# Performance work log

Measured on AMD Instinct MI355X. Metric: run time of the kernel, lower is better.

The kernel has to match this reference:

```python
import jax, jax.numpy as jnp
import numpy as np

I16_MIN, I16_MAX = -32768, 32767
NUM_SEG = 8


def setup_inputs() -> dict:
    key = jax.random.key(0)
    k1, k2, k3, k4, k5, k6 = jax.random.split(key, 6)
    # Float activation; quantized to qint16 inside the op via input_scale.
    x = jax.random.normal(k1, (16, 1024, 2048), dtype=jnp.float32)
    input_scale = jnp.full((1,), 1.0 / 8192.0, dtype=jnp.float32)  # randn*8192 spans most of int16
    out_scale = jnp.full((1,), 1e-3, dtype=jnp.float32)
    # Per-segment fixed-point linear coefficients (as produced by _convert_linear_kb / toqint):
    # 16-bit k, wide b pre-shifted by left_shift, result right-shifted by right_shift.
    alpha = jax.random.randint(k2, (NUM_SEG,), -4096, 4096, dtype=jnp.int32)        # int16 k
    beta = jax.random.randint(k3, (NUM_SEG,), -(1 << 20), 1 << 20, dtype=jnp.int32)  # int b
    left_shift = jax.random.randint(k4, (NUM_SEG,), 0, 5, dtype=jnp.int32)           # int8 shift
    right_shift = jax.random.randint(k5, (NUM_SEG,), 1, 15, dtype=jnp.int32)         # int8 shift
    # Sorted segment upper bounds in quantized domain; last entry pinned to qint16 max
    # (mirrors `segment_max[-1] = info.max` in _init_multi_table_params).
    segment_max = jnp.sort(jax.random.randint(k6, (NUM_SEG,), I16_MIN, I16_MAX, dtype=jnp.int32))
    segment_max = segment_max.at[-1].set(I16_MAX)
    return dict(x=x, input_scale=input_scale, out_scale=out_scale, alpha=alpha,
                beta=beta, left_shift=left_shift, right_shift=right_shift,
                segment_max=segment_max)


def reference(x, input_scale, out_scale, alpha, beta, left_shift, right_shift, segment_max):
    # Quantize input to qint16 (scale-only, zero_point = 0 as in the module).
    xi = jnp.clip(jnp.round(x / input_scale), I16_MIN, I16_MAX).astype(jnp.int32)
    # Segment selection: element belongs to the first segment whose upper bound >= xi.
    idx = jnp.clip(jnp.searchsorted(segment_max, xi, side='left'), 0, NUM_SEG - 1)
    # Gather per-segment fixed-point coefficients.
    k = alpha[idx]
    b = beta[idx]
    ls = left_shift[idx]
    rs = right_shift[idx]
    # Hardware shift-multiply-add: acc = k*x + (b << left_shift), then rounded
    # arithmetic right shift by right_shift, saturate to qint16.
    acc = k * xi + jnp.left_shift(b, ls)
    round_bias = jnp.where(rs > 0, jnp.left_shift(jnp.int32(1), jnp.maximum(rs - 1, 0)), jnp.int32(0))
    qy = jnp.clip(jnp.right_shift(acc + round_bias, rs), I16_MIN, I16_MAX)
    # Dequantized output (QTensor data * out_scale, zero_point = 0).
    return qy.astype(jnp.float32) * out_scale
```

## Files before the change

### kernel.cpp

```cpp
#include <hip/hip_runtime.h>


typedef float f32x4 __attribute__((ext_vector_type(4)));

__device__ __forceinline__ float seg_one(float x, float inv_s,
                                         float sm0, float sm1, float sm2, float sm3,
                                         float sm4, float sm5, float sm6,
                                         const float2* tab, float olo, float ohi)
{
    float xf = rintf(x * inv_s);
    xf = __builtin_amdgcn_fmed3f(xf, -32768.0f, 32767.0f);
    int idx = (sm0 < xf) + (sm1 < xf) + (sm2 < xf) + (sm3 < xf)
            + (sm4 < xf) + (sm5 < xf) + (sm6 < xf);
    float2 t = tab[idx];
    float y = fmaf(t.x, xf, t.y);
    return __builtin_amdgcn_fmed3f(y, olo, ohi);
}

__global__ __launch_bounds__(256) void SegmentLUT_83021717831949_kernel(
    const float* __restrict__ x,
    const float* __restrict__ input_scale,
    const float* __restrict__ out_scale,
    const int*   __restrict__ alpha,
    const int*   __restrict__ beta,
    const int*   __restrict__ lsh,
    const int*   __restrict__ rsh,
    const int*   __restrict__ smax,
    float*       __restrict__ out,
    int n)
{
    int nvec = n >> 2;
    int i = (int)(blockIdx.x * blockDim.x + threadIdx.x);
    bool valid = i < nvec;

    const f32x4* __restrict__ xv = (const f32x4*)x;
    f32x4 v = {};
    if (valid) v = xv[i];

    __shared__ float2 tab[8];
    float os = out_scale[0];
    if (threadIdx.x < 8) {
        int j  = (int)threadIdx.x;
        int rs = rsh[j];
        int rm1 = rs - 1 > 0 ? rs - 1 : 0;
        int rbias = rs > 0 ? (1 << rm1) : 0;
        int bc = (int)((unsigned)beta[j] << (lsh[j] & 31)) + rbias;
        float sc = ldexpf(os, -rs);
        tab[j] = make_float2((float)alpha[j] * sc, (float)bc * sc);
    }
    float inv_s = 1.0f / input_scale[0];
    float sm0 = (float)smax[0], sm1 = (float)smax[1], sm2 = (float)smax[2];
    float sm3 = (float)smax[3], sm4 = (float)smax[4], sm5 = (float)smax[5];
    float sm6 = (float)smax[6];
    float olo = -32768.0f * os, ohi = 32767.0f * os;
    __syncthreads();

    if (valid) {
        f32x4 o;
        o.x = seg_one(v.x, inv_s, sm0, sm1, sm2, sm3, sm4, sm5, sm6, tab, olo, ohi);
        o.y = seg_one(v.y, inv_s, sm0, sm1, sm2, sm3, sm4, sm5, sm6, tab, olo, ohi);
        o.z = seg_one(v.z, inv_s, sm0, sm1, sm2, sm3, sm4, sm5, sm6, tab, olo, ohi);
        o.w = seg_one(v.w, inv_s, sm0, sm1, sm2, sm3, sm4, sm5, sm6, tab, olo, ohi);
        ((f32x4*)out)[i] = o;
    }
    int ntail = n & 3;
    if (ntail && i < ntail) {
        int k = (nvec << 2) + i;
        out[k] = seg_one(x[k], inv_s, sm0, sm1, sm2, sm3, sm4, sm5, sm6, tab, olo, ohi);
    }
}

extern "C" void kernel_launch(void* const* d_in, const int* in_sizes, int n_in,
                              void* d_out, int out_size, void* d_ws, size_t ws_size,
                              hipStream_t stream) {
    const float* x           = (const float*)d_in[0];
    const float* input_scale = (const float*)d_in[1];
    const float* out_scale   = (const float*)d_in[2];
    const int*   alpha       = (const int*)d_in[3];
    const int*   beta        = (const int*)d_in[4];
    const int*   lsh         = (const int*)d_in[5];
    const int*   rsh         = (const int*)d_in[6];
    const int*   smax        = (const int*)d_in[7];
    float* out = (float*)d_out;

    int n = in_sizes[0];
    int nvec = n >> 2;
    int blocks = (nvec + 255) / 256;
    if (blocks < 1) blocks = 1;

    SegmentLUT_83021717831949_kernel<<<blocks, 256, 0, stream>>>(
        x, input_scale, out_scale, alpha, beta, lsh, rsh, smax, out, n);
}
```

Before: 228.6 us.

## Precompute segment table in a prep kernel and select coefficients with register selects

Adds a tiny one-block prep kernel that writes the fused per-segment slope/intercept table, the inverse input scale, the output clamp bounds and the float segment bounds into workspace. The main kernel loads these as uniform values, with no shared memory and no __syncthreads. Coefficients are now picked by a chain of compare-and-select instructions in registers instead of an indexed LDS lookup. This removes per-block table setup and the barrier, at the cost of one extra kernel launch and more VALU selects per element.

```diff
diff --git a/kernel.cpp b/kernel.cpp
--- a/kernel.cpp
+++ b/kernel.cpp
@@ -3,22 +3,7 @@
 
 typedef float f32x4 __attribute__((ext_vector_type(4)));
 
-__device__ __forceinline__ float seg_one(float x, float inv_s,
-                                         float sm0, float sm1, float sm2, float sm3,
-                                         float sm4, float sm5, float sm6,
-                                         const float2* tab, float olo, float ohi)
-{
-    float xf = rintf(x * inv_s);
-    xf = __builtin_amdgcn_fmed3f(xf, -32768.0f, 32767.0f);
-    int idx = (sm0 < xf) + (sm1 < xf) + (sm2 < xf) + (sm3 < xf)
-            + (sm4 < xf) + (sm5 < xf) + (sm6 < xf);
-    float2 t = tab[idx];
-    float y = fmaf(t.x, xf, t.y);
-    return __builtin_amdgcn_fmed3f(y, olo, ohi);
-}
-
-__global__ __launch_bounds__(256) void SegmentLUT_83021717831949_kernel(
-    const float* __restrict__ x,
+__global__ void SegmentLUT_83021717831949_prep(
     const float* __restrict__ input_scale,
     const float* __restrict__ out_scale,
     const int*   __restrict__ alpha,
@@ -26,47 +11,73 @@
     const int*   __restrict__ lsh,
     const int*   __restrict__ rsh,
     const int*   __restrict__ smax,
-    float*       __restrict__ out,
-    int n)
+    float*       __restrict__ ws)
 {
-    int nvec = n >> 2;
-    int i = (int)(blockIdx.x * blockDim.x + threadIdx.x);
-    bool valid = i < nvec;
-
-    const f32x4* __restrict__ xv = (const f32x4*)x;
-    f32x4 v = {};
-    if (valid) v = xv[i];
-
-    __shared__ float2 tab[8];
+    int j = (int)threadIdx.x;
     float os = out_scale[0];
-    if (threadIdx.x < 8) {
-        int j  = (int)threadIdx.x;
+    if (j < 8) {
         int rs = rsh[j];
         int rm1 = rs - 1 > 0 ? rs - 1 : 0;
         int rbias = rs > 0 ? (1 << rm1) : 0;
         int bc = (int)((unsigned)beta[j] << (lsh[j] & 31)) + rbias;
         float sc = ldexpf(os, -rs);
-        tab[j] = make_float2((float)alpha[j] * sc, (float)bc * sc);
+        ws[2 * j]     = (float)alpha[j] * sc;
+        ws[2 * j + 1] = (float)bc * sc;
     }
-    float inv_s = 1.0f / input_scale[0];
-    float sm0 = (float)smax[0], sm1 = (float)smax[1], sm2 = (float)smax[2];
-    float sm3 = (float)smax[3], sm4 = (float)smax[4], sm5 = (float)smax[5];
-    float sm6 = (float)smax[6];
-    float olo = -32768.0f * os, ohi = 32767.0f * os;
-    __syncthreads();
+    if (j == 8)  ws[16] = 1.0f / input_scale[0];
+    if (j == 9)  ws[17] = -32768.0f * os;
+    if (j == 10) ws[18] =  32767.0f * os;
+    if (j >= 11 && j < 18) ws[19 + (j - 11)] = (float)smax[j - 11];
+}
 
-    if (valid) {
+__global__ __launch_bounds__(256) void SegmentLUT_83021717831949_kernel(
+    const float* __restrict__ x,
+    const float* __restrict__ ws,
+    float*       __restrict__ out,
+    int n)
+{
+    float kf[8], bf[8];
+#pragma unroll
+    for (int j = 0; j < 8; ++j) { kf[j] = ws[2 * j]; bf[j] = ws[2 * j + 1]; }
+    float inv_s = ws[16], olo = ws[17], ohi = ws[18];
+    float smf[7];
+#pragma unroll
+    for (int j = 0; j < 7; ++j) smf[j] = ws[19 + j];
+
+    int nvec = n >> 2;
+    int i = (int)(blockIdx.x * blockDim.x + threadIdx.x);
+
+    if (i < nvec) {
+        f32x4 v = ((const f32x4*)x)[i];
         f32x4 o;
-        o.x = seg_one(v.x, inv_s, sm0, sm1, sm2, sm3, sm4, sm5, sm6, tab, olo, ohi);
-        o.y = seg_one(v.y, inv_s, sm0, sm1, sm2, sm3, sm4, sm5, sm6, tab, olo, ohi);
-        o.z = seg_one(v.z, inv_s, sm0, sm1, sm2, sm3, sm4, sm5, sm6, tab, olo, ohi);
-        o.w = seg_one(v.w, inv_s, sm0, sm1, sm2, sm3, sm4, sm5, sm6, tab, olo, ohi);
+#pragma unroll
+        for (int c = 0; c < 4; ++c) {
+            float xf = rintf(v[c] * inv_s);
+            xf = __builtin_amdgcn_fmed3f(xf, -32768.0f, 32767.0f);
+            float k = kf[7], b = bf[7];
+#pragma unroll
+            for (int j = 6; j >= 0; --j) {
+                bool csel = xf <= smf[j];
+                k = csel ? kf[j] : k;
+                b = csel ? bf[j] : b;
+            }
+            o[c] = __builtin_amdgcn_fmed3f(fmaf(k, xf, b), olo, ohi);
+        }
         ((f32x4*)out)[i] = o;
     }
     int ntail = n & 3;
     if (ntail && i < ntail) {
-        int k = (nvec << 2) + i;
-        out[k] = seg_one(x[k], inv_s, sm0, sm1, sm2, sm3, sm4, sm5, sm6, tab, olo, ohi);
+        int kidx = (nvec << 2) + i;
+        float xf = rintf(x[kidx] * inv_s);
+        xf = __builtin_amdgcn_fmed3f(xf, -32768.0f, 32767.0f);
+        float k = kf[7], b = bf[7];
+#pragma unroll
+        for (int j = 6; j >= 0; --j) {
+            bool csel = xf <= smf[j];
+            k = csel ? kf[j] : k;
+            b = csel ? bf[j] : b;
+        }
+        out[kidx] = __builtin_amdgcn_fmed3f(fmaf(k, xf, b), olo, ohi);
     }
 }
 
@@ -82,12 +93,15 @@
     const int*   rsh         = (const int*)d_in[6];
     const int*   smax        = (const int*)d_in[7];
     float* out = (float*)d_out;
+    float* ws  = (float*)d_ws;
 
     int n = in_sizes[0];
     int nvec = n >> 2;
     int blocks = (nvec + 255) / 256;
     if (blocks < 1) blocks = 1;
 
+    SegmentLUT_83021717831949_prep<<<1, 64, 0, stream>>>(
+        input_scale, out_scale, alpha, beta, lsh, rsh, smax, ws);
     SegmentLUT_83021717831949_kernel<<<blocks, 256, 0, stream>>>(
-        x, input_scale, out_scale, alpha, beta, lsh, rsh, smax, out, n);
+        x, ws, out, n);
 }
```

Measured after the change: 239.0 us. +4.6%, slower.
